# Performance work log

Hardware: AMD Instinct MI355X
Metric: run time of the kernel (lower is better)

The kernel has to match this reference:

```python
import jax, jax.numpy as jnp
import numpy as np

B, S, D, H = 4, 2048, 1024, 16
HD = D // H


def setup_inputs() -> dict:
    key = jax.random.key(0)
    k1, k2, k3 = jax.random.split(key, 3)
    hidden_states = jax.random.normal(k1, (B, S, D), dtype=jnp.float32)
    # torch nn.Linear weights: [out_features, in_features], no bias
    w_qkv = jax.random.normal(k2, (3 * D, D), dtype=jnp.float32) * (D ** -0.5)
    w_out = jax.random.normal(k3, (D, D), dtype=jnp.float32) * (D ** -0.5)
    attention_mask = jnp.ones((B, S), dtype=bool)  # True = attend
    # causal mask: True = masked (strict upper triangle)
    causal_mask = jnp.triu(jnp.ones((S, S), dtype=bool), k=1)[None, None, :, :]
    return {
        "hidden_states": hidden_states,
        "w_qkv": w_qkv,
        "w_out": w_out,
        "attention_mask": attention_mask,
        "causal_mask": causal_mask,
    }


def reference(hidden_states, w_qkv, w_out, attention_mask, causal_mask):
    b, s, d = hidden_states.shape
    scale = HD ** -0.5
    qkv = hidden_states @ w_qkv.T                      # [B,S,3D]
    qkv = qkv.reshape(b, s, 3, H, HD)
    qkv = jnp.transpose(qkv, (2, 0, 3, 1, 4))          # [3,B,H,S,HD]
    q, k, v = qkv[0], qkv[1], qkv[2]
    scores = jnp.einsum("bhqd,bhkd->bhqk", q, k) * scale
    scores = jnp.where(causal_mask, -jnp.inf, scores)
    key_mask = ~attention_mask[:, None, None, :]       # [B,1,1,S], True = masked
    scores = jnp.where(key_mask, -jnp.inf, scores)
    attn = jax.nn.softmax(scores, axis=-1)             # dropout: eval mode (identity)
    out = jnp.einsum("bhqk,bhkd->bhqd", attn, v)       # [B,H,S,HD]
    out = jnp.transpose(out, (0, 2, 1, 3)).reshape(b, s, d)
    return out @ w_out.T
```

## Files before the change

### kernel.cpp

```cpp
#include <hip/hip_runtime.h>

#define B_ 4
#define S_ 2048
#define D_ 1024
#define H_ 16
#define HD_ 64
#define QKV_LD (3*D_)
#define NEG_BIG (-1e30f)
#define PSCALE 0.18033688f
#define PSHIFT 11.5415603f

typedef __bf16 bf16x8 __attribute__((ext_vector_type(8)));
typedef float f32x4 __attribute__((ext_vector_type(4)));
typedef float f32x16 __attribute__((ext_vector_type(16)));

__device__ __forceinline__ unsigned short f2bf(float f) {
    union { float f; unsigned int u; } v; v.f = f;
    return (unsigned short)((v.u + 0x8000u) >> 16);
}

__device__ __forceinline__ unsigned pack_bf(float a, float b) {
    union { float f; unsigned u; } x, y; x.f = a; y.f = b;
    return __builtin_amdgcn_perm(y.u + 0x8000u, x.u + 0x8000u, 0x07060302u);
}

__device__ __forceinline__ void glds16(const unsigned short* g, unsigned short* l) {
    __builtin_amdgcn_global_load_lds(
        (const __attribute__((address_space(1))) unsigned int*)g,
        (__attribute__((address_space(3))) unsigned int*)l, 16, 0, 0);
}

__device__ __forceinline__ void cvt8(const float* s, unsigned short* d, int j) {
    const float4 f0 = *(const float4*)(s + (size_t)j * 8);
    const float4 f1 = *(const float4*)(s + (size_t)j * 8 + 4);
    uint4 o;
    o.x = pack_bf(f0.x, f0.y); o.y = pack_bf(f0.z, f0.w);
    o.z = pack_bf(f1.x, f1.y); o.w = pack_bf(f1.z, f1.w);
    *(uint4*)(d + (size_t)j * 8) = o;
}

__global__ __launch_bounds__(256) void cvt_bf16(const float* __restrict__ src,
                                                unsigned short* __restrict__ dst, int n8) {
    int i = blockIdx.x * 256 + threadIdx.x;
    if (i < n8) cvt8(src, dst, i);
}

__global__ __launch_bounds__(256) void cvt_fused(const float* __restrict__ s0, unsigned short* __restrict__ d0, int n0,
                                                 const float* __restrict__ s1, unsigned short* __restrict__ d1, int n1,
                                                 const float* __restrict__ s2, unsigned short* __restrict__ d2, int n2) {
    int i = blockIdx.x * 256 + threadIdx.x;
    if (i < n0)                  cvt8(s0, d0, i);
    else if (i - n0 < n1)        cvt8(s1, d1, i - n0);
    else if (i - n0 - n1 < n2)   cvt8(s2, d2, i - n0 - n1);
}

#define AFRAG(dst, base, row_) do { const int r_ = (row_); \
    dst = *(const bf16x8*)((const char*)(base) + r_*64 + ((l4*16) ^ (((r_>>1)&3)<<4))); } while (0)

#define STG(reg, c) do { \
    glds16(Ag0 + (size_t)(c)*32, LAw + (reg)*4096); \
    glds16(Ag1 + (size_t)(c)*32, LAw + (reg)*4096 + 2048); \
    glds16(Bg0 + (size_t)(c)*32, LBw + (reg)*4096); \
    glds16(Bg1 + (size_t)(c)*32, LBw + (reg)*4096 + 2048); } while (0)

#define PH(reg, STAGECODE, WAITCODE) do { \
    _Pragma("unroll") \
    for (int q = 0; q < 4; ++q) \
        AFRAG(a_[q], LA + (reg)*4096, wm*64 + q*16 + l15); \
    _Pragma("unroll") \
    for (int q = 0; q < 4; ++q) \
        AFRAG(b_[q], LB + (reg)*4096, wn*64 + q*16 + l15); \
    STAGECODE; \
    WAITCODE; \
    __builtin_amdgcn_sched_barrier(0); \
    __builtin_amdgcn_s_barrier(); \
    asm volatile("s_waitcnt lgkmcnt(0)" ::: "memory"); \
    __builtin_amdgcn_sched_barrier(0); \
    __builtin_amdgcn_s_setprio(1); \
    _Pragma("unroll") \
    for (int q = 0; q < 4; ++q) { \
        _Pragma("unroll") \
        for (int n_ = 0; n_ < 4; ++n_) \
            acc[q][n_] = __builtin_amdgcn_mfma_f32_16x16x32_bf16(a_[q], b_[n_], acc[q][n_], 0, 0, 0); \
    } \
    __builtin_amdgcn_s_setprio(0); \
    __builtin_amdgcn_sched_barrier(0); \
    __builtin_amdgcn_s_barrier(); \
} while (0)

template<int CF32>
__global__ __launch_bounds__(256, 2) void gemm8p(const unsigned short* __restrict__ A,
                                                 const unsigned short* __restrict__ W,
                                                 void* __restrict__ Cp,
                                                 int M, int N, int K)
{
    __shared__ unsigned short lds[32768];
    unsigned short* LA = lds;
    unsigned short* LB = lds + 16384;

    const int tid = threadIdx.x;
    const int wave = tid >> 6, lane = tid & 63;
    const int l15 = lane & 15, l4 = lane >> 4;
    const int wm = wave >> 1, wn = wave & 1;

    const int nbx = N >> 7;
    const int nwg = nbx * (M >> 7);
    const int wg0 = blockIdx.y * gridDim.x + blockIdx.x;
    const int wg  = (wg0 & 7) * (nwg >> 3) + (wg0 >> 3);
    const int n0 = (wg % nbx) * 128, m0 = (wg / nbx) * 128;

    const int lrow = tid >> 2;
    const int cswz = ((tid & 3) * 16) ^ (((lrow >> 1) & 3) << 4);
    const unsigned short* Ag0 = A + (size_t)(m0 + lrow) * K + (cswz >> 1);
    const unsigned short* Ag1 = Ag0 + (size_t)64 * K;
    const unsigned short* Bg0 = W + (size_t)(n0 + lrow) * K + (cswz >> 1);
    const unsigned short* Bg1 = Bg0 + (size_t)64 * K;
    unsigned short* LAw = LA + wave * 512;
    unsigned short* LBw = LB + wave * 512;

    const f32x4 fzero = {0.f, 0.f, 0.f, 0.f};
    f32x4 acc[4][4];
    #pragma unroll
    for (int i = 0; i < 4; ++i)
        #pragma unroll
        for (int j = 0; j < 4; ++j) acc[i][j] = fzero;

    STG(0, 0); STG(1, 1); STG(2, 2);
    asm volatile("s_waitcnt vmcnt(8)" ::: "memory");
    __builtin_amdgcn_s_barrier();

    const int niter = K >> 7;
    for (int i = 0; i < niter; ++i) {
        bf16x8 a_[4], b_[4];
        const int c0 = 4 * i;
        const bool st = (i < niter - 1);

        PH(0, { STG(3, c0 + 3); },
              { asm volatile("s_waitcnt vmcnt(8)" ::: "memory"); });
        PH(1, { if (st) STG(0, c0 + 4); },
              { if (st) asm volatile("s_waitcnt vmcnt(8)" ::: "memory");
                else    asm volatile("s_waitcnt vmcnt(4)" ::: "memory"); });
        PH(2, { if (st) STG(1, c0 + 5); },
              { if (st) asm volatile("s_waitcnt vmcnt(8)" ::: "memory");
                else    asm volatile("s_waitcnt vmcnt(0)" ::: "memory"); });
        PH(3, { if (st) STG(2, c0 + 6); },
              { if (st) asm volatile("s_waitcnt vmcnt(8)" ::: "memory"); });
    }

    #pragma unroll
    for (int mi = 0; mi < 4; ++mi)
        #pragma unroll
        for (int ni = 0; ni < 4; ++ni)
            #pragma unroll
            for (int r = 0; r < 4; ++r) {
                int m = m0 + wm*64 + mi*16 + l4*4 + r;
                int n = n0 + wn*64 + ni*16 + l15;
                if (CF32) ((float*)Cp)[(size_t)m * N + n] = acc[mi][ni][r];
                else      ((unsigned short*)Cp)[(size_t)m * N + n] = f2bf(acc[mi][ni][r]);
            }
}

__global__ __launch_bounds__(256, 4) void attn_fwd(const unsigned short* __restrict__ qkv,
                                                   unsigned short* __restrict__ out)
{
    __shared__ unsigned short Qs [128*72];
    __shared__ unsigned short Ks [64*72];
    __shared__ unsigned short Vts[64*72];

    const int tid  = threadIdx.x;
    const int wave = tid >> 6, lane = tid & 63;
    const int l31 = lane & 31, l5 = lane >> 5;
    const int qb = 15 - blockIdx.y;
    const int bh = blockIdx.x;
    const int b = bh >> 4, h = bh & 15;
    const int q0 = qb * 128;

    const unsigned short* Qg = qkv + (size_t)b * S_ * QKV_LD + h * HD_;
    const unsigned short* Kg = Qg + D_;
    const unsigned short* Vg = Qg + 2 * D_;

    #pragma unroll
    for (int i = 0; i < 4; ++i) {
        int lin = i * 256 + tid;
        int r = lin >> 3, c = (lin & 7) * 8;
        *(uint4*)&Qs[r * 72 + c] = *(const uint4*)&Qg[(size_t)(q0 + r) * QKV_LD + c];
    }
    __syncthreads();
    bf16x8 aq[4];
    #pragma unroll
    for (int db = 0; db < 4; ++db)
        aq[db] = *(const bf16x8*)&Qs[(wave*32 + l31) * 72 + db*16 + l5*8];

    f32x16 oacc[2];
    #pragma unroll
    for (int nb = 0; nb < 2; ++nb)
        #pragma unroll
        for (int r = 0; r < 16; ++r) oacc[nb][r] = 0.f;
    float lsum = 0.f;

    const int kr = tid >> 3, kc8 = (tid & 7) * 8;
    const int dg = tid & 7;
    const int colv = (2*kr + 16*(dg >> 1)) & 63;
    const int wq0 = q0 + wave * 32;
    const int jmax = 2 * qb + 1;

    uint4 kq0 = *(const uint4*)&Kg[(size_t)kr * QKV_LD + kc8];
    uint4 kq1 = *(const uint4*)&Kg[(size_t)(32 + kr) * QKV_LD + kc8];
    uint4 vq0 = *(const uint4*)&Vg[(size_t)(2*kr)     * QKV_LD + dg*8];
    uint4 vq1 = *(const uint4*)&Vg[(size_t)(2*kr + 1) * QKV_LD + dg*8];

    for (int j = 0; j <= jmax; ++j) {
        __syncthreads();
        *(uint4*)&Ks[kr * 72 + kc8]        = kq0;
        *(uint4*)&Ks[(32 + kr) * 72 + kc8] = kq1;
        {
            union { uint4 q; unsigned w[4]; } v0, v1;
            v0.q = vq0; v1.q = vq1;
            #pragma unroll
            for (int w = 0; w < 4; ++w) {
                unsigned lo = __builtin_amdgcn_perm(v1.w[w], v0.w[w], 0x05040100u);
                unsigned hi = __builtin_amdgcn_perm(v1.w[w], v0.w[w], 0x07060302u);
                *(unsigned*)&Vts[(dg*8 + 2*w)     * 72 + colv] = lo;
                *(unsigned*)&Vts[(dg*8 + 2*w + 1) * 72 + colv] = hi;
            }
        }
        __syncthreads();

        if (j < jmax) {
            const size_t k0n = (size_t)(j + 1) * 64;
            kq0 = *(const uint4*)&Kg[(k0n + kr) * QKV_LD + kc8];
            kq1 = *(const uint4*)&Kg[(k0n + 32 + kr) * QKV_LD + kc8];
            vq0 = *(const uint4*)&Vg[(k0n + 2*kr)     * QKV_LD + dg*8];
            vq1 = *(const uint4*)&Vg[(k0n + 2*kr + 1) * QKV_LD + dg*8];
        }

        if (64 * j < wq0 + 32) {
            const bool bnd = (64 * (j + 1) > wq0);
            const int off = wq0 - 64 * j;
            unsigned pk[16];

            #pragma unroll
            for (int kblk = 0; kblk < 2; ++kblk) {
                f32x16 s;
                #pragma unroll
                for (int r = 0; r < 16; ++r) s[r] = 0.f;
                __builtin_amdgcn_s_setprio(1);
                #pragma unroll
                for (int db = 0; db < 4; ++db) {
                    bf16x8 kb = *(const bf16x8*)&Ks[(kblk*32 + l31) * 72 + db*16 + l5*8];
                    s = __builtin_amdgcn_mfma_f32_32x32x16_bf16(kb, aq[db], s, 0, 0, 0);
                }
                __builtin_amdgcn_s_setprio(0);
                if (bnd) {
                    #pragma unroll
                    for (int r = 0; r < 16; ++r) {
                        int kl = kblk*32 + (r & 3) + 8*(r >> 2) + 4*l5;
                        if (kl > off + l31) s[r] = NEG_BIG;
                    }
                }
                float p[16];
                #pragma unroll
                for (int r = 0; r < 16; ++r)
                    p[r] = __builtin_exp2f(s[r] * PSCALE - PSHIFT);
                lsum += (((p[0]+p[1]) + (p[2]+p[3])) + ((p[4]+p[5]) + (p[6]+p[7])))
                      + (((p[8]+p[9]) + (p[10]+p[11])) + ((p[12]+p[13]) + (p[14]+p[15])));
                #pragma unroll
                for (int jj = 0; jj < 8; ++jj)
                    pk[kblk*8 + jj] = pack_bf(p[2*jj], p[2*jj+1]);
            }

            __builtin_amdgcn_s_setprio(1);
            #pragma unroll
            for (int kc4 = 0; kc4 < 4; ++kc4) {
                const int j0 = (kc4 >> 1)*8 + (kc4 & 1)*4;
                unsigned a0 = pk[j0],   b0 = pk[j0+2];
                unsigned a1 = pk[j0+1], b1 = pk[j0+3];
                asm("v_permlane32_swap_b32 %0, %1" : "+v"(a0), "+v"(b0));
                asm("v_permlane32_swap_b32 %0, %1" : "+v"(a1), "+v"(b1));
                union { unsigned u[4]; bf16x8 v; } af;
                af.u[0] = a0; af.u[1] = a1; af.u[2] = b0; af.u[3] = b1;
                #pragma unroll
                for (int nb = 0; nb < 2; ++nb) {
                    const int colb = (kc4*16 + l5*8 + nb*32 + (l31 >> 4)*16) & 63;
                    bf16x8 bv = *(const bf16x8*)&Vts[(nb*32 + l31) * 72 + colb];
                    oacc[nb] = __builtin_amdgcn_mfma_f32_32x32x16_bf16(af.v, bv, oacc[nb], 0, 0, 0);
                }
            }
            __builtin_amdgcn_s_setprio(0);
        }
    }

    lsum += __shfl_xor(lsum, 32);
    const float inv = (lsum > 0.f) ? (1.0f / lsum) : 0.f;
    #pragma unroll
    for (int r = 0; r < 16; ++r) {
        const int rowof = (r & 3) + 8*(r >> 2) + 4*l5;
        const float invq = __shfl(inv, rowof);
        const int q = q0 + wave*32 + rowof;
        const size_t base = ((size_t)b * S_ + q) * D_ + h * HD_;
        out[base + l31]      = f2bf(oacc[0][r] * invq);
        out[base + 32 + l31] = f2bf(oacc[1][r] * invq);
    }
}

extern "C" void kernel_launch(void* const* d_in, const int* in_sizes, int n_in,
                              void* d_out, int out_size, void* d_ws, size_t ws_size,
                              hipStream_t stream)
{
    const float* hidden = (const float*)d_in[0];
    const float* w_qkv  = (const float*)d_in[1];
    const float* w_out  = (const float*)d_in[2];

    const int M = B_ * S_;

    unsigned short* qkv_ws  = (unsigned short*)d_ws;
    unsigned short* attn_ws = qkv_ws + (size_t)M * 3 * D_;
    unsigned short* Hb = attn_ws;
    unsigned short* Wq = (unsigned short*)d_out;

    const int n0 = M*D_/8, n1 = 3*D_*D_/8, n2 = D_*D_/8;
    const size_t need = ((size_t)M*3*D_ + (size_t)M*D_ + (size_t)D_*D_) * 2;

    if (ws_size >= need) {
        unsigned short* Wo = attn_ws + (size_t)M * D_;
        cvt_fused<<<(n0+n1+n2+255)/256, 256, 0, stream>>>(hidden, Hb, n0,
                                                          w_qkv,  Wq, n1,
                                                          w_out,  Wo, n2);
        gemm8p<0><<<dim3(3*D_/128, M/128), 256, 0, stream>>>(Hb, Wq, qkv_ws, M, 3*D_, D_);
        attn_fwd<<<dim3(B_*H_, S_/128), 256, 0, stream>>>(qkv_ws, attn_ws);
        gemm8p<1><<<dim3(D_/128, M/128), 256, 0, stream>>>(attn_ws, Wo, d_out, M, D_, D_);
    } else {
        unsigned short* Wo = qkv_ws;
        cvt_fused<<<(n0+n1+255)/256, 256, 0, stream>>>(hidden, Hb, n0,
                                                       w_qkv,  Wq, n1,
                                                       (const float*)0, (unsigned short*)0, 0);
        gemm8p<0><<<dim3(3*D_/128, M/128), 256, 0, stream>>>(Hb, Wq, qkv_ws, M, 3*D_, D_);
        attn_fwd<<<dim3(B_*H_, S_/128), 256, 0, stream>>>(qkv_ws, attn_ws);
        cvt_bf16<<<(n2+255)/256, 256, 0, stream>>>(w_out, Wo, n2);
        gemm8p<1><<<dim3(D_/128, M/128), 256, 0, stream>>>(attn_ws, Wo, d_out, M, D_, D_);
    }
}
```

Before: 252.9 us.

## Enlarge GEMM tiles to 256x128 with 8 waves and 3-stage K=64 pipeline

The bf16 GEMM now runs 512 threads per block computing a 256x128 output tile. Each stage covers K=64, with a 128-byte swizzled LDS row layout and three LDS buffers. The K loop is hard-coded to 16 tiles (K=1024), and each block has 144KB of LDS. The aim is more reuse of each B tile and fewer barriers per K step, at the cost of fewer resident blocks and K being baked into the loop.

```diff
diff --git a/kernel.cpp b/kernel.cpp
--- a/kernel.cpp
+++ b/kernel.cpp
@@ -54,22 +54,28 @@
     else if (i - n0 - n1 < n2)   cvt8(s2, d2, i - n0 - n1);
 }
 
-#define AFRAG(dst, base, row_) do { const int r_ = (row_); \
-    dst = *(const bf16x8*)((const char*)(base) + r_*64 + ((l4*16) ^ (((r_>>1)&3)<<4))); } while (0)
-
-#define STG(reg, c) do { \
-    glds16(Ag0 + (size_t)(c)*32, LAw + (reg)*4096); \
-    glds16(Ag1 + (size_t)(c)*32, LAw + (reg)*4096 + 2048); \
-    glds16(Bg0 + (size_t)(c)*32, LBw + (reg)*4096); \
-    glds16(Bg1 + (size_t)(c)*32, LBw + (reg)*4096 + 2048); } while (0)
-
-#define PH(reg, STAGECODE, WAITCODE) do { \
+#define VMW(n) asm volatile("s_waitcnt vmcnt(" #n ")" ::: "memory")
+
+#define AFR(dst, basep, row_, kk) do { const int r_ = (row_); \
+    dst = *(const bf16x8*)((const char*)(basep) + r_*128 + (((kk)*64 + l4*16) ^ ((r_&7)<<4))); } while (0)
+
+#define STG6(LAb, LBb, kt) do { \
+    glds16(Ag0 + (size_t)(kt)*64, (LAb) + wave*512); \
+    glds16(Ag1 + (size_t)(kt)*64, (LAb) + 4096  + wave*512); \
+    glds16(Ag2 + (size_t)(kt)*64, (LAb) + 8192  + wave*512); \
+    glds16(Ag3 + (size_t)(kt)*64, (LAb) + 12288 + wave*512); \
+    glds16(Bg0 + (size_t)(kt)*64, (LBb) + wave*512); \
+    glds16(Bg1 + (size_t)(kt)*64, (LBb) + 4096  + wave*512); } while (0)
+
+#define PH(LAb, LBb, STAGECODE, WAITCODE) do { \
+    bf16x8 a_[2][4], b_[2][4]; \
     _Pragma("unroll") \
-    for (int q = 0; q < 4; ++q) \
-        AFRAG(a_[q], LA + (reg)*4096, wm*64 + q*16 + l15); \
-    _Pragma("unroll") \
-    for (int q = 0; q < 4; ++q) \
-        AFRAG(b_[q], LB + (reg)*4096, wn*64 + q*16 + l15); \
+    for (int kk = 0; kk < 2; ++kk) { \
+        _Pragma("unroll") \
+        for (int q = 0; q < 4; ++q) AFR(a_[kk][q], (LAb), wm*64 + q*16 + l15, kk); \
+        _Pragma("unroll") \
+        for (int q = 0; q < 4; ++q) AFR(b_[kk][q], (LBb), wn*64 + q*16 + l15, kk); \
+    } \
     STAGECODE; \
     WAITCODE; \
     __builtin_amdgcn_sched_barrier(0); \
@@ -80,8 +86,10 @@
     _Pragma("unroll") \
     for (int q = 0; q < 4; ++q) { \
         _Pragma("unroll") \
-        for (int n_ = 0; n_ < 4; ++n_) \
-            acc[q][n_] = __builtin_amdgcn_mfma_f32_16x16x32_bf16(a_[q], b_[n_], acc[q][n_], 0, 0, 0); \
+        for (int n_ = 0; n_ < 4; ++n_) { \
+            acc[q][n_] = __builtin_amdgcn_mfma_f32_16x16x32_bf16(a_[0][q], b_[0][n_], acc[q][n_], 0, 0, 0); \
+            acc[q][n_] = __builtin_amdgcn_mfma_f32_16x16x32_bf16(a_[1][q], b_[1][n_], acc[q][n_], 0, 0, 0); \
+        } \
     } \
     __builtin_amdgcn_s_setprio(0); \
     __builtin_amdgcn_sched_barrier(0); \
@@ -89,14 +97,18 @@
 } while (0)
 
 template<int CF32>
-__global__ __launch_bounds__(256, 2) void gemm8p(const unsigned short* __restrict__ A,
+__global__ __launch_bounds__(512, 2) void gemm8p(const unsigned short* __restrict__ A,
                                                  const unsigned short* __restrict__ W,
                                                  void* __restrict__ Cp,
                                                  int M, int N, int K)
 {
-    __shared__ unsigned short lds[32768];
-    unsigned short* LA = lds;
-    unsigned short* LB = lds + 16384;
+    __shared__ unsigned short lds[73728];
+    unsigned short* const A0 = lds;
+    unsigned short* const A1 = lds + 16384;
+    unsigned short* const A2 = lds + 32768;
+    unsigned short* const B0 = lds + 49152;
+    unsigned short* const B1 = lds + 57344;
+    unsigned short* const B2 = lds + 65536;
 
     const int tid = threadIdx.x;
     const int wave = tid >> 6, lane = tid & 63;
@@ -104,19 +116,19 @@
     const int wm = wave >> 1, wn = wave & 1;
 
     const int nbx = N >> 7;
-    const int nwg = nbx * (M >> 7);
+    const int nwg = nbx * (M >> 8);
     const int wg0 = blockIdx.y * gridDim.x + blockIdx.x;
     const int wg  = (wg0 & 7) * (nwg >> 3) + (wg0 >> 3);
-    const int n0 = (wg % nbx) * 128, m0 = (wg / nbx) * 128;
-
-    const int lrow = tid >> 2;
-    const int cswz = ((tid & 3) * 16) ^ (((lrow >> 1) & 3) << 4);
-    const unsigned short* Ag0 = A + (size_t)(m0 + lrow) * K + (cswz >> 1);
-    const unsigned short* Ag1 = Ag0 + (size_t)64 * K;
-    const unsigned short* Bg0 = W + (size_t)(n0 + lrow) * K + (cswz >> 1);
+    const int n0 = (wg % nbx) * 128, m0 = (wg / nbx) * 256;
+
+    const int srow = tid >> 3;
+    const int scol = (((tid & 7) * 16) ^ ((srow & 7) << 4)) >> 1;
+    const unsigned short* Ag0 = A + (size_t)(m0 + srow) * K + scol;
+    const unsigned short* Ag1 = Ag0 + (size_t)64  * K;
+    const unsigned short* Ag2 = Ag0 + (size_t)128 * K;
+    const unsigned short* Ag3 = Ag0 + (size_t)192 * K;
+    const unsigned short* Bg0 = W + (size_t)(n0 + srow) * K + scol;
     const unsigned short* Bg1 = Bg0 + (size_t)64 * K;
-    unsigned short* LAw = LA + wave * 512;
-    unsigned short* LBw = LB + wave * 512;
 
     const f32x4 fzero = {0.f, 0.f, 0.f, 0.f};
     f32x4 acc[4][4];
@@ -125,27 +137,19 @@
         #pragma unroll
         for (int j = 0; j < 4; ++j) acc[i][j] = fzero;
 
-    STG(0, 0); STG(1, 1); STG(2, 2);
-    asm volatile("s_waitcnt vmcnt(8)" ::: "memory");
+    STG6(A0, B0, 0);
+    STG6(A1, B1, 1);
+    VMW(6);
     __builtin_amdgcn_s_barrier();
 
-    const int niter = K >> 7;
-    for (int i = 0; i < niter; ++i) {
-        bf16x8 a_[4], b_[4];
-        const int c0 = 4 * i;
-        const bool st = (i < niter - 1);
-
-        PH(0, { STG(3, c0 + 3); },
-              { asm volatile("s_waitcnt vmcnt(8)" ::: "memory"); });
-        PH(1, { if (st) STG(0, c0 + 4); },
-              { if (st) asm volatile("s_waitcnt vmcnt(8)" ::: "memory");
-                else    asm volatile("s_waitcnt vmcnt(4)" ::: "memory"); });
-        PH(2, { if (st) STG(1, c0 + 5); },
-              { if (st) asm volatile("s_waitcnt vmcnt(8)" ::: "memory");
-                else    asm volatile("s_waitcnt vmcnt(0)" ::: "memory"); });
-        PH(3, { if (st) STG(2, c0 + 6); },
-              { if (st) asm volatile("s_waitcnt vmcnt(8)" ::: "memory"); });
-    }
+    for (int i = 0; i < 5; ++i) {
+        const int p = 3 * i;
+        PH(A0, B0, { STG6(A2, B2, p + 2); }, { VMW(6); });
+        PH(A1, B1, { STG6(A0, B0, p + 3); }, { VMW(6); });
+        PH(A2, B2, { if (i < 4) STG6(A1, B1, p + 4); },
+                   { if (i < 4) { VMW(6); } else { VMW(0); } });
+    }
+    PH(A0, B0, {}, {});
 
     #pragma unroll
     for (int mi = 0; mi < 4; ++mi)
@@ -326,17 +330,17 @@
         cvt_fused<<<(n0+n1+n2+255)/256, 256, 0, stream>>>(hidden, Hb, n0,
                                                           w_qkv,  Wq, n1,
                                                           w_out,  Wo, n2);
-        gemm8p<0><<<dim3(3*D_/128, M/128), 256, 0, stream>>>(Hb, Wq, qkv_ws, M, 3*D_, D_);
+        gemm8p<0><<<dim3(3*D_/128, M/256), 512, 0, stream>>>(Hb, Wq, qkv_ws, M, 3*D_, D_);
         attn_fwd<<<dim3(B_*H_, S_/128), 256, 0, stream>>>(qkv_ws, attn_ws);
-        gemm8p<1><<<dim3(D_/128, M/128), 256, 0, stream>>>(attn_ws, Wo, d_out, M, D_, D_);
+        gemm8p<1><<<dim3(D_/128, M/256), 512, 0, stream>>>(attn_ws, Wo, d_out, M, D_, D_);
     } else {
         unsigned short* Wo = qkv_ws;
         cvt_fused<<<(n0+n1+255)/256, 256, 0, stream>>>(hidden, Hb, n0,
                                                        w_qkv,  Wq, n1,
                                                        (const float*)0, (unsigned short*)0, 0);
-        gemm8p<0><<<dim3(3*D_/128, M/128), 256, 0, stream>>>(Hb, Wq, qkv_ws, M, 3*D_, D_);
+        gemm8p<0><<<dim3(3*D_/128, M/256), 512, 0, stream>>>(Hb, Wq, qkv_ws, M, 3*D_, D_);
         attn_fwd<<<dim3(B_*H_, S_/128), 256, 0, stream>>>(qkv_ws, attn_ws);
         cvt_bf16<<<(n2+255)/256, 256, 0, stream>>>(w_out, Wo, n2);
-        gemm8p<1><<<dim3(D_/128, M/128), 256, 0, stream>>>(attn_ws, Wo, d_out, M, D_, D_);
-    }
-}
+        gemm8p<1><<<dim3(D_/128, M/256), 512, 0, stream>>>(attn_ws, Wo, d_out, M, D_, D_);
+    }
+}
```

Measured after the change: 255.1 us. About the same (+0.9%).

## Split attention KV range across two wave groups with shared-memory merge

Applied to the files above, without the earlier changes.

Each attention block now has 512 threads in two groups of four waves. Each group processes half of the causal key-block range for the same 128 query rows, using its own K/V shared-memory buffers. Because the softmax uses a fixed shift and no running max, the partial outputs and row sums are simply added through shared memory before normalising and storing. This shortens each block's serial KV loop and raises parallelism for the long query blocks. The cost is extra shared memory, a merge step, and occupancy limited to two blocks per CU.

```diff
diff --git a/kernel.cpp b/kernel.cpp
--- a/kernel.cpp
+++ b/kernel.cpp
@@ -160,15 +160,21 @@
             }
 }
 
-__global__ __launch_bounds__(256, 4) void attn_fwd(const unsigned short* __restrict__ qkv,
+#define OFF_KS0  0
+#define OFF_VTS0 4608
+#define OFF_QS   9216
+#define OFF_KS1  18432
+#define OFF_VTS1 23040
+
+__global__ __launch_bounds__(512, 2) void attn_fwd(const unsigned short* __restrict__ qkv,
                                                    unsigned short* __restrict__ out)
 {
-    __shared__ unsigned short Qs [128*72];
-    __shared__ unsigned short Ks [64*72];
-    __shared__ unsigned short Vts[64*72];
+    __shared__ unsigned short smem[27648];
+    unsigned short* const Qs = smem + OFF_QS;
 
     const int tid  = threadIdx.x;
     const int wave = tid >> 6, lane = tid & 63;
+    const int wl = wave & 3, grp = wave >> 2;
     const int l31 = lane & 31, l5 = lane >> 5;
     const int qb = 15 - blockIdx.y;
     const int bh = blockIdx.x;
@@ -179,9 +185,12 @@
     const unsigned short* Kg = Qg + D_;
     const unsigned short* Vg = Qg + 2 * D_;
 
-    #pragma unroll
-    for (int i = 0; i < 4; ++i) {
-        int lin = i * 256 + tid;
+    unsigned short* const KsG  = smem + (grp ? OFF_KS1 : OFF_KS0);
+    unsigned short* const VtsG = smem + (grp ? OFF_VTS1 : OFF_VTS0);
+
+    #pragma unroll
+    for (int i = 0; i < 2; ++i) {
+        int lin = i * 512 + tid;
         int r = lin >> 3, c = (lin & 7) * 8;
         *(uint4*)&Qs[r * 72 + c] = *(const uint4*)&Qg[(size_t)(q0 + r) * QKV_LD + c];
     }
@@ -189,7 +198,7 @@
     bf16x8 aq[4];
     #pragma unroll
     for (int db = 0; db < 4; ++db)
-        aq[db] = *(const bf16x8*)&Qs[(wave*32 + l31) * 72 + db*16 + l5*8];
+        aq[db] = *(const bf16x8*)&Qs[(wl*32 + l31) * 72 + db*16 + l5*8];
 
     f32x16 oacc[2];
     #pragma unroll
@@ -198,21 +207,26 @@
         for (int r = 0; r < 16; ++r) oacc[nb][r] = 0.f;
     float lsum = 0.f;
 
-    const int kr = tid >> 3, kc8 = (tid & 7) * 8;
-    const int dg = tid & 7;
+    const int t = tid & 255;
+    const int kr = t >> 3, kc8 = (t & 7) * 8;
+    const int dg = t & 7;
     const int colv = (2*kr + 16*(dg >> 1)) & 63;
-    const int wq0 = q0 + wave * 32;
-    const int jmax = 2 * qb + 1;
-
-    uint4 kq0 = *(const uint4*)&Kg[(size_t)kr * QKV_LD + kc8];
-    uint4 kq1 = *(const uint4*)&Kg[(size_t)(32 + kr) * QKV_LD + kc8];
-    uint4 vq0 = *(const uint4*)&Vg[(size_t)(2*kr)     * QKV_LD + dg*8];
-    uint4 vq1 = *(const uint4*)&Vg[(size_t)(2*kr + 1) * QKV_LD + dg*8];
-
-    for (int j = 0; j <= jmax; ++j) {
+    const int wq0 = q0 + wl * 32;
+
+    const int j0    = grp ? (qb + 1) : 0;
+    const int niter = qb + 1;
+    const int jlast = grp ? (2*qb + 1) : qb;
+
+    uint4 kq0 = *(const uint4*)&Kg[((size_t)j0*64 + kr) * QKV_LD + kc8];
+    uint4 kq1 = *(const uint4*)&Kg[((size_t)j0*64 + 32 + kr) * QKV_LD + kc8];
+    uint4 vq0 = *(const uint4*)&Vg[((size_t)j0*64 + 2*kr)     * QKV_LD + dg*8];
+    uint4 vq1 = *(const uint4*)&Vg[((size_t)j0*64 + 2*kr + 1) * QKV_LD + dg*8];
+
+    for (int it = 0; it < niter; ++it) {
+        const int j = j0 + it;
         __syncthreads();
-        *(uint4*)&Ks[kr * 72 + kc8]        = kq0;
-        *(uint4*)&Ks[(32 + kr) * 72 + kc8] = kq1;
+        *(uint4*)&KsG[kr * 72 + kc8]        = kq0;
+        *(uint4*)&KsG[(32 + kr) * 72 + kc8] = kq1;
         {
             union { uint4 q; unsigned w[4]; } v0, v1;
             v0.q = vq0; v1.q = vq1;
@@ -220,13 +234,13 @@
             for (int w = 0; w < 4; ++w) {
                 unsigned lo = __builtin_amdgcn_perm(v1.w[w], v0.w[w], 0x05040100u);
                 unsigned hi = __builtin_amdgcn_perm(v1.w[w], v0.w[w], 0x07060302u);
-                *(unsigned*)&Vts[(dg*8 + 2*w)     * 72 + colv] = lo;
-                *(unsigned*)&Vts[(dg*8 + 2*w + 1) * 72 + colv] = hi;
+                *(unsigned*)&VtsG[(dg*8 + 2*w)     * 72 + colv] = lo;
+                *(unsigned*)&VtsG[(dg*8 + 2*w + 1) * 72 + colv] = hi;
             }
         }
         __syncthreads();
 
-        if (j < jmax) {
+        if (j < jlast) {
             const size_t k0n = (size_t)(j + 1) * 64;
             kq0 = *(const uint4*)&Kg[(k0n + kr) * QKV_LD + kc8];
             kq1 = *(const uint4*)&Kg[(k0n + 32 + kr) * QKV_LD + kc8];
@@ -247,7 +261,7 @@
                 __builtin_amdgcn_s_setprio(1);
                 #pragma unroll
                 for (int db = 0; db < 4; ++db) {
-                    bf16x8 kb = *(const bf16x8*)&Ks[(kblk*32 + l31) * 72 + db*16 + l5*8];
+                    bf16x8 kb = *(const bf16x8*)&KsG[(kblk*32 + l31) * 72 + db*16 + l5*8];
                     s = __builtin_amdgcn_mfma_f32_32x32x16_bf16(kb, aq[db], s, 0, 0, 0);
                 }
                 __builtin_amdgcn_s_setprio(0);
@@ -272,9 +286,9 @@
             __builtin_amdgcn_s_setprio(1);
             #pragma unroll
             for (int kc4 = 0; kc4 < 4; ++kc4) {
-                const int j0 = (kc4 >> 1)*8 + (kc4 & 1)*4;
-                unsigned a0 = pk[j0],   b0 = pk[j0+2];
-                unsigned a1 = pk[j0+1], b1 = pk[j0+3];
+                const int jp = (kc4 >> 1)*8 + (kc4 & 1)*4;
+                unsigned a0 = pk[jp],   b0 = pk[jp+2];
+                unsigned a1 = pk[jp+1], b1 = pk[jp+3];
                 asm("v_permlane32_swap_b32 %0, %1" : "+v"(a0), "+v"(b0));
                 asm("v_permlane32_swap_b32 %0, %1" : "+v"(a1), "+v"(b1));
                 union { unsigned u[4]; bf16x8 v; } af;
@@ -282,7 +296,7 @@
                 #pragma unroll
                 for (int nb = 0; nb < 2; ++nb) {
                     const int colb = (kc4*16 + l5*8 + nb*32 + (l31 >> 4)*16) & 63;
-                    bf16x8 bv = *(const bf16x8*)&Vts[(nb*32 + l31) * 72 + colb];
+                    bf16x8 bv = *(const bf16x8*)&VtsG[(nb*32 + l31) * 72 + colb];
                     oacc[nb] = __builtin_amdgcn_mfma_f32_32x32x16_bf16(af.v, bv, oacc[nb], 0, 0, 0);
                 }
             }
@@ -290,16 +304,40 @@
         }
     }
 
+    float* const mO = (float*)(smem + OFF_QS);
+    float* const mL = mO + 128*64;
+    __syncthreads();
     lsum += __shfl_xor(lsum, 32);
-    const float inv = (lsum > 0.f) ? (1.0f / lsum) : 0.f;
-    #pragma unroll
-    for (int r = 0; r < 16; ++r) {
-        const int rowof = (r & 3) + 8*(r >> 2) + 4*l5;
-        const float invq = __shfl(inv, rowof);
-        const int q = q0 + wave*32 + rowof;
-        const size_t base = ((size_t)b * S_ + q) * D_ + h * HD_;
-        out[base + l31]      = f2bf(oacc[0][r] * invq);
-        out[base + 32 + l31] = f2bf(oacc[1][r] * invq);
+    if (grp == 1) {
+        #pragma unroll
+        for (int r = 0; r < 16; ++r) {
+            const int rowof = (r & 3) + 8*(r >> 2) + 4*l5;
+            const int row = wl*32 + rowof;
+            mO[row*64 + l31]      = oacc[0][r];
+            mO[row*64 + 32 + l31] = oacc[1][r];
+        }
+        if (l5 == 0) mL[wl*32 + l31] = lsum;
+    }
+    __syncthreads();
+    if (grp == 0) {
+        #pragma unroll
+        for (int r = 0; r < 16; ++r) {
+            const int rowof = (r & 3) + 8*(r >> 2) + 4*l5;
+            const int row = wl*32 + rowof;
+            oacc[0][r] += mO[row*64 + l31];
+            oacc[1][r] += mO[row*64 + 32 + l31];
+        }
+        const float ltot = lsum + mL[wl*32 + l31];
+        const float inv = (ltot > 0.f) ? (1.0f / ltot) : 0.f;
+        #pragma unroll
+        for (int r = 0; r < 16; ++r) {
+            const int rowof = (r & 3) + 8*(r >> 2) + 4*l5;
+            const float invq = __shfl(inv, rowof);
+            const int q = q0 + wl*32 + rowof;
+            const size_t base = ((size_t)b * S_ + q) * D_ + h * HD_;
+            out[base + l31]      = f2bf(oacc[0][r] * invq);
+            out[base + 32 + l31] = f2bf(oacc[1][r] * invq);
+        }
     }
 }
 
@@ -327,7 +365,7 @@
                                                           w_qkv,  Wq, n1,
                                                           w_out,  Wo, n2);
         gemm8p<0><<<dim3(3*D_/128, M/128), 256, 0, stream>>>(Hb, Wq, qkv_ws, M, 3*D_, D_);
-        attn_fwd<<<dim3(B_*H_, S_/128), 256, 0, stream>>>(qkv_ws, attn_ws);
+        attn_fwd<<<dim3(B_*H_, 16), 512, 0, stream>>>(qkv_ws, attn_ws);
         gemm8p<1><<<dim3(D_/128, M/128), 256, 0, stream>>>(attn_ws, Wo, d_out, M, D_, D_);
     } else {
         unsigned short* Wo = qkv_ws;
@@ -335,7 +373,7 @@
                                                        w_qkv,  Wq, n1,
                                                        (const float*)0, (unsigned short*)0, 0);
         gemm8p<0><<<dim3(3*D_/128, M/128), 256, 0, stream>>>(Hb, Wq, qkv_ws, M, 3*D_, D_);
-        attn_fwd<<<dim3(B_*H_, S_/128), 256, 0, stream>>>(qkv_ws, attn_ws);
+        attn_fwd<<<dim3(B_*H_, 16), 512, 0, stream>>>(qkv_ws, attn_ws);
         cvt_bf16<<<(n2+255)/256, 256, 0, stream>>>(w_out, Wo, n2);
         gemm8p<1><<<dim3(D_/128, M/128), 256, 0, stream>>>(attn_ws, Wo, d_out, M, D_, D_);
     }
```

Measured after the change: 267.5 us. 5.8% more time.

## Fuse hidden-state fp32-to-bf16 conversion into QKV GEMM operand staging

Applied to the files above, without the earlier changes.

Adds a new QKV GEMM kernel that stages fp32 hidden-state tiles into LDS directly and converts them to bf16 when forming MFMA A fragments. The separate conversion pass over the 8M-element activation tensor and its bf16 write and reread are dropped. In exchange the GEMM moves twice as many A bytes per tile, uses a larger LDS footprint (96KB, one block per CU), and repeats the conversion work across N-tiles. It also adds a grouped workgroup remap for cache locality.

```diff
diff --git a/kernel.cpp b/kernel.cpp
--- a/kernel.cpp
+++ b/kernel.cpp
@@ -30,6 +30,12 @@
         (__attribute__((address_space(3))) unsigned int*)l, 16, 0, 0);
 }
 
+__device__ __forceinline__ void glds16f(const float* g, unsigned short* l) {
+    __builtin_amdgcn_global_load_lds(
+        (const __attribute__((address_space(1))) unsigned int*)g,
+        (__attribute__((address_space(3))) unsigned int*)l, 16, 0, 0);
+}
+
 __device__ __forceinline__ void cvt8(const float* s, unsigned short* d, int j) {
     const float4 f0 = *(const float4*)(s + (size_t)j * 8);
     const float4 f1 = *(const float4*)(s + (size_t)j * 8 + 4);
@@ -52,6 +58,122 @@
     if (i < n0)                  cvt8(s0, d0, i);
     else if (i - n0 < n1)        cvt8(s1, d1, i - n0);
     else if (i - n0 - n1 < n2)   cvt8(s2, d2, i - n0 - n1);
+}
+
+#define VMW(n) asm volatile("s_waitcnt vmcnt(" #n ")" ::: "memory")
+
+#define AFRAGF(dst, reg, row_) do { const int r_ = (row_); \
+    const int b0_ = (l4*32) ^ ((r_&7)<<4); \
+    const char* bp_ = (const char*)lds + (reg)*16384 + r_*128; \
+    const float4 lo_ = *(const float4*)(bp_ + b0_); \
+    const float4 hi_ = *(const float4*)(bp_ + (b0_^16)); \
+    union { unsigned u[4]; bf16x8 v; } cv_; \
+    cv_.u[0] = pack_bf(lo_.x, lo_.y); cv_.u[1] = pack_bf(lo_.z, lo_.w); \
+    cv_.u[2] = pack_bf(hi_.x, hi_.y); cv_.u[3] = pack_bf(hi_.z, hi_.w); \
+    dst = cv_.v; } while (0)
+
+#define BFRAGF(dst, reg, row_) do { const int r_ = (row_); \
+    dst = *(const bf16x8*)((const char*)lds + 65536 + (reg)*8192 + r_*64 + ((l4*16) ^ (((r_>>1)&3)<<4))); } while (0)
+
+#define STG_AF(reg, c) do { \
+    glds16f(Ag0 + (size_t)(c)*32, lds + (reg)*8192 + wave*512); \
+    glds16f(Ag1 + (size_t)(c)*32, lds + (reg)*8192 + 2048 + wave*512); \
+    glds16f(Ag2 + (size_t)(c)*32, lds + (reg)*8192 + 4096 + wave*512); \
+    glds16f(Ag3 + (size_t)(c)*32, lds + (reg)*8192 + 6144 + wave*512); } while (0)
+#define STG_BF(reg, c) do { \
+    glds16(Bg0 + (size_t)(c)*32, lds + 32768 + (reg)*4096 + wave*512); \
+    glds16(Bg1 + (size_t)(c)*32, lds + 32768 + (reg)*4096 + 2048 + wave*512); } while (0)
+
+#define PHF(reg, STAGECODE, WAITCODE) do { \
+    bf16x8 a_[4], b_[4]; \
+    _Pragma("unroll") \
+    for (int q = 0; q < 4; ++q) AFRAGF(a_[q], reg, wm*64 + q*16 + l15); \
+    _Pragma("unroll") \
+    for (int q = 0; q < 4; ++q) BFRAGF(b_[q], reg, wn*64 + q*16 + l15); \
+    STAGECODE; \
+    WAITCODE; \
+    __builtin_amdgcn_sched_barrier(0); \
+    __builtin_amdgcn_s_barrier(); \
+    asm volatile("s_waitcnt lgkmcnt(0)" ::: "memory"); \
+    __builtin_amdgcn_sched_barrier(0); \
+    __builtin_amdgcn_s_setprio(1); \
+    _Pragma("unroll") \
+    for (int q = 0; q < 4; ++q) { \
+        _Pragma("unroll") \
+        for (int n_ = 0; n_ < 4; ++n_) \
+            acc[q][n_] = __builtin_amdgcn_mfma_f32_16x16x32_bf16(a_[q], b_[n_], acc[q][n_], 0, 0, 0); \
+    } \
+    __builtin_amdgcn_s_setprio(0); \
+    __builtin_amdgcn_sched_barrier(0); \
+    __builtin_amdgcn_s_barrier(); \
+} while (0)
+
+__global__ __launch_bounds__(256, 1) void gemm_qkvf(const float* __restrict__ A,
+                                                    const unsigned short* __restrict__ W,
+                                                    unsigned short* __restrict__ Cp,
+                                                    int M, int N, int K)
+{
+    __shared__ unsigned short lds[49152];
+
+    const int tid = threadIdx.x;
+    const int wave = tid >> 6, lane = tid & 63;
+    const int l15 = lane & 15, l4 = lane >> 4;
+    const int wm = wave >> 1, wn = wave & 1;
+
+    const int nbx = N >> 7;
+    const int nwg = nbx * (M >> 7);
+    const int wg0 = blockIdx.y * gridDim.x + blockIdx.x;
+    const int wg  = (wg0 & 7) * (nwg >> 3) + (wg0 >> 3);
+    const int n0 = (wg % nbx) * 128, m0 = (wg / nbx) * 128;
+
+    const int arow = tid >> 3;
+    const int gslot = (tid & 7) ^ (arow & 7);
+    const float* Ag0 = A + (size_t)(m0 + arow) * K + gslot * 4;
+    const float* Ag1 = Ag0 + (size_t)32 * K;
+    const float* Ag2 = Ag0 + (size_t)64 * K;
+    const float* Ag3 = Ag0 + (size_t)96 * K;
+    const int brow = tid >> 2;
+    const int bswz = ((tid & 3) * 16) ^ (((brow >> 1) & 3) << 4);
+    const unsigned short* Bg0 = W + (size_t)(n0 + brow) * K + (bswz >> 1);
+    const unsigned short* Bg1 = Bg0 + (size_t)64 * K;
+
+    const f32x4 fzero = {0.f, 0.f, 0.f, 0.f};
+    f32x4 acc[4][4];
+    #pragma unroll
+    for (int i = 0; i < 4; ++i)
+        #pragma unroll
+        for (int j = 0; j < 4; ++j) acc[i][j] = fzero;
+
+    STG_AF(0, 0); STG_BF(0, 0);
+    STG_AF(1, 1); STG_BF(1, 1);
+    STG_AF(2, 2); STG_BF(2, 2);
+    VMW(12);
+    __builtin_amdgcn_s_barrier();
+
+    const int niter = K >> 7;
+    for (int i = 0; i < niter; ++i) {
+        const int c0 = 4 * i;
+        const bool st = (i < niter - 1);
+
+        PHF(0, { STG_AF(3, c0 + 3); STG_BF(3, c0 + 3); }, { VMW(12); });
+        PHF(1, { if (st) { STG_AF(0, c0 + 4); STG_BF(0, c0 + 4); } },
+               { if (st) { VMW(12); } else { VMW(6); } });
+        PHF(2, { if (st) { STG_AF(1, c0 + 5); STG_BF(1, c0 + 5); } },
+               { if (st) { VMW(12); } else { VMW(0); } });
+        PHF(3, { if (st) { STG_AF(2, c0 + 6); STG_BF(2, c0 + 6); } },
+               { if (st) { VMW(12); } });
+    }
+
+    #pragma unroll
+    for (int mi = 0; mi < 4; ++mi)
+        #pragma unroll
+        for (int ni = 0; ni < 4; ++ni)
+            #pragma unroll
+            for (int r = 0; r < 4; ++r) {
+                int m = m0 + wm*64 + mi*16 + l4*4 + r;
+                int n = n0 + wn*64 + ni*16 + l15;
+                Cp[(size_t)m * N + n] = f2bf(acc[mi][ni][r]);
+            }
 }
 
 #define AFRAG(dst, base, row_) do { const int r_ = (row_); \
@@ -126,7 +248,7 @@
         for (int j = 0; j < 4; ++j) acc[i][j] = fzero;
 
     STG(0, 0); STG(1, 1); STG(2, 2);
-    asm volatile("s_waitcnt vmcnt(8)" ::: "memory");
+    VMW(8);
     __builtin_amdgcn_s_barrier();
 
     const int niter = K >> 7;
@@ -135,16 +257,13 @@
         const int c0 = 4 * i;
         const bool st = (i < niter - 1);
 
-        PH(0, { STG(3, c0 + 3); },
-              { asm volatile("s_waitcnt vmcnt(8)" ::: "memory"); });
+        PH(0, { STG(3, c0 + 3); }, { VMW(8); });
         PH(1, { if (st) STG(0, c0 + 4); },
-              { if (st) asm volatile("s_waitcnt vmcnt(8)" ::: "memory");
-                else    asm volatile("s_waitcnt vmcnt(4)" ::: "memory"); });
+              { if (st) { VMW(8); } else { VMW(4); } });
         PH(2, { if (st) STG(1, c0 + 5); },
-              { if (st) asm volatile("s_waitcnt vmcnt(8)" ::: "memory");
-                else    asm volatile("s_waitcnt vmcnt(0)" ::: "memory"); });
+              { if (st) { VMW(8); } else { VMW(0); } });
         PH(3, { if (st) STG(2, c0 + 6); },
-              { if (st) asm volatile("s_waitcnt vmcnt(8)" ::: "memory"); });
+              { if (st) { VMW(8); } });
     }
 
     #pragma unroll
@@ -315,26 +434,25 @@
 
     unsigned short* qkv_ws  = (unsigned short*)d_ws;
     unsigned short* attn_ws = qkv_ws + (size_t)M * 3 * D_;
-    unsigned short* Hb = attn_ws;
     unsigned short* Wq = (unsigned short*)d_out;
 
-    const int n0 = M*D_/8, n1 = 3*D_*D_/8, n2 = D_*D_/8;
+    const int n1 = 3*D_*D_/8, n2 = D_*D_/8;
     const size_t need = ((size_t)M*3*D_ + (size_t)M*D_ + (size_t)D_*D_) * 2;
 
     if (ws_size >= need) {
         unsigned short* Wo = attn_ws + (size_t)M * D_;
-        cvt_fused<<<(n0+n1+n2+255)/256, 256, 0, stream>>>(hidden, Hb, n0,
-                                                          w_qkv,  Wq, n1,
-                                                          w_out,  Wo, n2);
-        gemm8p<0><<<dim3(3*D_/128, M/128), 256, 0, stream>>>(Hb, Wq, qkv_ws, M, 3*D_, D_);
+        cvt_fused<<<(n1+n2+255)/256, 256, 0, stream>>>(w_qkv, Wq, n1,
+                                                       w_out, Wo, n2,
+                                                       (const float*)0, (unsigned short*)0, 0);
+        gemm_qkvf<<<dim3(3*D_/128, M/128), 256, 0, stream>>>(hidden, Wq, qkv_ws, M, 3*D_, D_);
         attn_fwd<<<dim3(B_*H_, S_/128), 256, 0, stream>>>(qkv_ws, attn_ws);
         gemm8p<1><<<dim3(D_/128, M/128), 256, 0, stream>>>(attn_ws, Wo, d_out, M, D_, D_);
     } else {
         unsigned short* Wo = qkv_ws;
-        cvt_fused<<<(n0+n1+255)/256, 256, 0, stream>>>(hidden, Hb, n0,
-                                                       w_qkv,  Wq, n1,
-                                                       (const float*)0, (unsigned short*)0, 0);
-        gemm8p<0><<<dim3(3*D_/128, M/128), 256, 0, stream>>>(Hb, Wq, qkv_ws, M, 3*D_, D_);
+        cvt_fused<<<(n1+255)/256, 256, 0, stream>>>(w_qkv, Wq, n1,
+                                                    (const float*)0, (unsigned short*)0, 0,
+                                                    (const float*)0, (unsigned short*)0, 0);
+        gemm_qkvf<<<dim3(3*D_/128, M/128), 256, 0, stream>>>(hidden, Wq, qkv_ws, M, 3*D_, D_);
         attn_fwd<<<dim3(B_*H_, S_/128), 256, 0, stream>>>(qkv_ws, attn_ws);
         cvt_bf16<<<(n2+255)/256, 256, 0, stream>>>(w_out, Wo, n2);
         gemm8p<1><<<dim3(D_/128, M/128), 256, 0, stream>>>(attn_ws, Wo, d_out, M, D_, D_);
```

After: 320.8 us. 26.9% more time.
